# Kernel tuning notes

Hardware: AMD Instinct MI355X
Metric: run time of the kernel (lower is better)

The kernel has to match this reference:

```python
import jax, jax.numpy as jnp
import numpy as np

VOCAB, EMB, HID, OUT = 32000, 512, 1024, 1
B, S = 128, 512


def setup_inputs() -> dict:
    key = jax.random.key(0)
    ks = jax.random.split(key, 8)
    x = jax.random.randint(ks[0], (B, S), 0, VOCAB, dtype=jnp.int64 if jax.config.jax_enable_x64 else jnp.int32)
    emb = jax.random.normal(ks[1], (VOCAB, EMB), dtype=jnp.float32)
    # torch Linear stores weight as [out, in], y = x @ W.T + b
    W_w = jax.random.normal(ks[2], (HID, EMB), dtype=jnp.float32) * (1.0 / np.sqrt(EMB))
    W_b = jax.random.normal(ks[3], (HID,), dtype=jnp.float32) * 0.01
    U_w = jax.random.normal(ks[4], (HID, HID), dtype=jnp.float32) * (1.0 / np.sqrt(HID))
    U_b = jax.random.normal(ks[5], (HID,), dtype=jnp.float32) * 0.01
    V_w = jax.random.normal(ks[6], (OUT, HID), dtype=jnp.float32) * (1.0 / np.sqrt(HID))
    V_b = jax.random.normal(ks[7], (OUT,), dtype=jnp.float32) * 0.01
    return {"x": x, "emb": emb, "W_w": W_w, "W_b": W_b, "U_w": U_w, "U_b": U_b, "V_w": V_w, "V_b": V_b}


def reference(x, emb, W_w, W_b, U_w, U_b, V_w, V_b):
    xe = emb[x]  # [B, S, E] embedding lookup
    # Precompute input projection for all timesteps (same math as per-step W(x_t))
    pre = jnp.einsum('bse,he->bsh', xe, W_w) + W_b  # [B, S, H]

    def step(h, p_t):
        # h_t = tanh(W x_t + b_W + U h_{t-1} + b_U)
        h_new = jnp.tanh(p_t + h @ U_w.T + U_b)
        return h_new, None

    h0 = jnp.zeros((x.shape[0], U_w.shape[0]), dtype=pre.dtype)
    hT, _ = jax.lax.scan(step, h0, jnp.swapaxes(pre, 0, 1))  # scan over seq
    logits = hT @ V_w.T + V_b  # [B, OUT]
    return jax.nn.sigmoid(logits)
```

## Files before the change

kernel.cpp:

```cpp
#include <hip/hip_runtime.h>
#include <hip/hip_bf16.h>

typedef short short8 __attribute__((ext_vector_type(8)));
typedef float f32x4 __attribute__((ext_vector_type(4)));

#define OFF_U   0x0UL
#define OFF_W   0x200000UL
#define OFF_PRE 0x300000UL
#define OFF_H0  0x8300000UL
#define OFF_H1  0x8340000UL
#define OFF_CNT 0x8380000UL

static __device__ __forceinline__ unsigned short f2bf(float f) {
  return __builtin_bit_cast(unsigned short, __float2bfloat16(f));
}
static __device__ __forceinline__ float bf2f(unsigned short u) {
  unsigned int v = (unsigned int)u << 16;
  return __builtin_bit_cast(float, v);
}
static __device__ __forceinline__ unsigned int pack2(float a, float b) {
  return (unsigned int)f2bf(a) | ((unsigned int)f2bf(b) << 16);
}
static __device__ __forceinline__ float fast_tanh(float x) {
  float xc = fminf(fmaxf(x, -10.f), 10.f);
  float e2 = __expf(2.f * xc);
  return 1.f - 2.f * __builtin_amdgcn_rcpf(e2 + 1.f);
}

__global__ __launch_bounds__(256) void cvt_bf16(const float* __restrict__ in,
                                                unsigned short* __restrict__ out, int n4) {
  int idx = blockIdx.x * 256 + threadIdx.x;
  if (idx < n4) {
    float4 v = *(const float4*)&in[idx * 4];
    uint2 p; p.x = pack2(v.x, v.y); p.y = pack2(v.z, v.w);
    *(uint2*)&out[idx * 4] = p;
  }
}

__global__ __launch_bounds__(256) void pre_gemm(const int* __restrict__ x,
                                                const float* __restrict__ emb,
                                                const unsigned short* __restrict__ Wbf,
                                                unsigned short* __restrict__ pre) {
  const int t   = blockIdx.y;
  const int n0  = blockIdx.x * 128;
  const int tid = threadIdx.x;
  const int lane = tid & 63, w = tid >> 6;
  const int q = lane >> 4, l15 = lane & 15;

  __shared__ unsigned short Alds[128][72];
  __shared__ unsigned short Blds[128][72];
  __shared__ int tok[128];
  if (tid < 128) tok[tid] = x[tid * 512 + t];
  __syncthreads();

  f32x4 acc[4][4];
  #pragma unroll
  for (int a = 0; a < 4; ++a)
    #pragma unroll
    for (int b = 0; b < 4; ++b) acc[a][b] = {0.f, 0.f, 0.f, 0.f};

  const int wm = (w & 1) * 64, wn = (w >> 1) * 64;

  for (int k0 = 0; k0 < 512; k0 += 64) {
    #pragma unroll
    for (int it = 0; it < 8; ++it) {
      int idx = it * 256 + tid;
      int r = idx >> 4, c4 = (idx & 15) * 4;
      float4 v = *(const float4*)&emb[tok[r] * 512 + k0 + c4];
      uint2 p; p.x = pack2(v.x, v.y); p.y = pack2(v.z, v.w);
      *(uint2*)&Alds[r][c4] = p;
    }
    #pragma unroll
    for (int it = 0; it < 4; ++it) {
      int idx = it * 256 + tid;
      int r = idx >> 3, c8 = (idx & 7) * 8;
      *(int4*)&Blds[r][c8] = *(const int4*)&Wbf[(n0 + r) * 512 + k0 + c8];
    }
    __syncthreads();
    #pragma unroll
    for (int kt = 0; kt < 2; ++kt) {
      short8 af[4], bfr[4];
      #pragma unroll
      for (int mt = 0; mt < 4; ++mt) af[mt]  = *(const short8*)&Alds[wm + mt*16 + l15][kt*32 + q*8];
      #pragma unroll
      for (int nt = 0; nt < 4; ++nt) bfr[nt] = *(const short8*)&Blds[wn + nt*16 + l15][kt*32 + q*8];
      #pragma unroll
      for (int mt = 0; mt < 4; ++mt)
        #pragma unroll
        for (int nt = 0; nt < 4; ++nt)
          acc[mt][nt] = __builtin_amdgcn_mfma_f32_16x16x32_bf16(af[mt], bfr[nt], acc[mt][nt], 0, 0, 0);
    }
    __syncthreads();
  }
  #pragma unroll
  for (int mt = 0; mt < 4; ++mt) {
    int brow = wm + mt * 16 + q * 4;
    #pragma unroll
    for (int nt = 0; nt < 4; ++nt) {
      int i = n0 + wn + nt * 16 + l15;
      #pragma unroll
      for (int r = 0; r < 4; ++r)
        pre[(t * 128 + brow + r) * 1024 + i] = f2bf(acc[mt][nt][r]);
    }
  }
}

__global__ __launch_bounds__(512, 2) void recurrence(const unsigned short* __restrict__ Ubf,
                                                     const unsigned short* __restrict__ pre,
                                                     const float* __restrict__ Wb,
                                                     const float* __restrict__ Ub,
                                                     unsigned short* __restrict__ h0buf,
                                                     unsigned short* __restrict__ h1buf,
                                                     unsigned int* __restrict__ cnt) {
  const int c   = blockIdx.x & 7;
  const int s   = blockIdx.x >> 3;
  const int tid = threadIdx.x;
  const int lane = tid & 63, wv = tid >> 6;
  const int q = lane >> 4, l15 = lane & 15;
  const int ibase = s * 128 + wv * 16;
  const int bglob = c * 16;

  __shared__ unsigned short hlds[16][1032];

  short8 A[32];
  {
    const unsigned short* Up = Ubf + (ibase + l15) * 1024 + q * 8;
    #pragma unroll
    for (int kt = 0; kt < 32; ++kt) A[kt] = *(const short8*)(Up + kt * 32);
  }
  #pragma unroll
  for (int kt = 0; kt < 32; ++kt) asm volatile("" : "+v"(A[kt]));

  float4 bias;
  {
    int i0 = ibase + q * 4;
    float4 wb = *(const float4*)&Wb[i0];
    float4 ub = *(const float4*)&Ub[i0];
    bias = make_float4(wb.x + ub.x, wb.y + ub.y, wb.z + ub.z, wb.w + ub.w);
  }

  unsigned int* fbase = cnt + c * 32;
  const unsigned int* fpoll = fbase + (lane & 7);
  unsigned int* fmine = fbase + s;
  const int sb = tid >> 7;
  const int sk = (tid & 127) * 8;
  const unsigned short* prebase = pre + (size_t)(bglob + l15) * 1024 + ibase + q * 4;

  #pragma unroll 1
  for (int t = 0; t < 512; ++t) {
    ushort4 pv = *(const ushort4*)(prebase + (size_t)t * 131072);

    const unsigned short* hprev = (t & 1) ? h1buf : h0buf;
    unsigned short* hnew        = (t & 1) ? h0buf : h1buf;

    if (t > 0) {
      if (wv == 0) {
        const unsigned int tt = (unsigned int)t;
        for (;;) {
          unsigned int v;
          asm volatile("global_load_dword %0, %1, off sc1\n\ts_waitcnt vmcnt(0)"
                       : "=v"(v) : "v"(fpoll));
          if (__ballot(v < tt) == 0) break;
        }
      }
      __syncthreads();
    }

    {
      const unsigned short* hp = hprev + (size_t)(bglob + sb) * 1024 + sk;
      int4 r0, r1, r2, r3;
      asm volatile(
        "global_load_dwordx4 %0, %4, off sc1\n\t"
        "global_load_dwordx4 %1, %5, off sc1\n\t"
        "global_load_dwordx4 %2, %6, off sc1\n\t"
        "global_load_dwordx4 %3, %7, off sc1\n\t"
        "s_waitcnt vmcnt(0)"
        : "=&v"(r0), "=&v"(r1), "=&v"(r2), "=&v"(r3)
        : "v"(hp), "v"(hp + 4 * 1024), "v"(hp + 8 * 1024), "v"(hp + 12 * 1024));
      *(int4*)&hlds[sb][sk]      = r0;
      *(int4*)&hlds[sb + 4][sk]  = r1;
      *(int4*)&hlds[sb + 8][sk]  = r2;
      *(int4*)&hlds[sb + 12][sk] = r3;
    }
    __syncthreads();

    f32x4 acc0 = {0.f, 0.f, 0.f, 0.f}, acc1 = {0.f, 0.f, 0.f, 0.f};
    #pragma unroll
    for (int kt = 0; kt < 32; kt += 2) {
      short8 b0 = *(const short8*)&hlds[l15][kt * 32 + q * 8];
      short8 b1 = *(const short8*)&hlds[l15][kt * 32 + 32 + q * 8];
      acc0 = __builtin_amdgcn_mfma_f32_16x16x32_bf16(A[kt],     b0, acc0, 0, 0, 0);
      acc1 = __builtin_amdgcn_mfma_f32_16x16x32_bf16(A[kt + 1], b1, acc1, 0, 0, 0);
    }

    float x0 = acc0[0] + acc1[0] + bf2f(pv.x) + bias.x;
    float x1 = acc0[1] + acc1[1] + bf2f(pv.y) + bias.y;
    float x2 = acc0[2] + acc1[2] + bf2f(pv.z) + bias.z;
    float x3 = acc0[3] + acc1[3] + bf2f(pv.w) + bias.w;
    uint2 pk;
    pk.x = pack2(fast_tanh(x0), fast_tanh(x1));
    pk.y = pack2(fast_tanh(x2), fast_tanh(x3));

    {
      unsigned short* dst = hnew + (size_t)(bglob + l15) * 1024 + ibase + q * 4;
      asm volatile("global_store_dwordx2 %0, %1, off sc1\n\ts_waitcnt vmcnt(0)"
                   : : "v"(dst), "v"(pk));
    }
    __syncthreads();
    if (tid == 0) {
      unsigned int tv = (unsigned int)(t + 1);
      asm volatile("global_store_dword %0, %1, off sc1\n\ts_waitcnt vmcnt(0)"
                   : : "v"(fmine), "v"(tv));
    }
  }
}

__global__ __launch_bounds__(64) void final_out(const unsigned short* __restrict__ hT,
                                                const float* __restrict__ Vw,
                                                const float* __restrict__ Vb,
                                                float* __restrict__ out) {
  int b = blockIdx.x, lane = threadIdx.x;
  float sum = 0.f;
  #pragma unroll
  for (int k = 0; k < 16; ++k) {
    int i = k * 64 + lane;
    sum += bf2f(hT[b * 1024 + i]) * Vw[i];
  }
  #pragma unroll
  for (int off = 32; off; off >>= 1) sum += __shfl_down(sum, off);
  if (lane == 0) out[b] = 1.f / (1.f + expf(-(sum + Vb[0])));
}

extern "C" void kernel_launch(void* const* d_in, const int* in_sizes, int n_in,
                              void* d_out, int out_size, void* d_ws, size_t ws_size,
                              hipStream_t stream) {
  const int*   x   = (const int*)d_in[0];
  const float* emb = (const float*)d_in[1];
  const float* W_w = (const float*)d_in[2];
  const float* W_b = (const float*)d_in[3];
  const float* U_w = (const float*)d_in[4];
  const float* U_b = (const float*)d_in[5];
  const float* V_w = (const float*)d_in[6];
  const float* V_b = (const float*)d_in[7];
  float* out = (float*)d_out;
  char*  ws  = (char*)d_ws;

  unsigned short* Ubf = (unsigned short*)(ws + OFF_U);
  unsigned short* Wbf = (unsigned short*)(ws + OFF_W);
  unsigned short* pre = (unsigned short*)(ws + OFF_PRE);
  unsigned short* h0  = (unsigned short*)(ws + OFF_H0);
  unsigned short* h1  = (unsigned short*)(ws + OFF_H1);
  unsigned int*   cnt = (unsigned int*)(ws + OFF_CNT);

  hipMemsetAsync(ws + OFF_H0, 0, (OFF_CNT - OFF_H0) + 0x1000, stream);

  cvt_bf16<<<1024, 256, 0, stream>>>(U_w, Ubf, 1024 * 1024 / 4);
  cvt_bf16<<<512, 256, 0, stream>>>(W_w, Wbf, 1024 * 512 / 4);

  pre_gemm<<<dim3(8, 512), 256, 0, stream>>>(x, emb, Wbf, pre);

  void* args[] = {&Ubf, &pre, &W_b, &U_b, &h0, &h1, &cnt};
  hipLaunchCooperativeKernel((void*)recurrence, dim3(64), dim3(512), args, 0, stream);

  final_out<<<128, 64, 0, stream>>>(h0, V_w, V_b, out);
}
```

Measured before the change: 1.724 ms.

## Keep own h slice in LDS, pipeline flag polling, skip own-slice reload

Each block now writes its freshly computed h slice directly into LDS and reloads only the other blocks' slices from global memory. Flag polling skips the block's own flag and keeps two loads in flight instead of one. The pre load is issued early without waiting, and the final flag store no longer waits for completion. The goal is to shorten the per-timestep critical path of the cross-block recurrence. The cost is an extra __syncthreads per step, added so LDS is not overwritten while other waves still read it.

```diff
diff --git a/kernel.cpp b/kernel.cpp
--- a/kernel.cpp
+++ b/kernel.cpp
@@ -122,6 +122,12 @@
 
   __shared__ unsigned short hlds[16][1032];
 
+  {
+    int r = tid >> 5;
+    int kk = (tid & 31) * 4;
+    *(uint2*)&hlds[r][s * 128 + kk] = make_uint2(0u, 0u);
+  }
+
   short8 A[32];
   {
     const unsigned short* Up = Ubf + (ibase + l15) * 1024 + q * 8;
@@ -140,15 +146,23 @@
   }
 
   unsigned int* fbase = cnt + c * 32;
+  const bool pact = (lane < 8) && (lane != s);
   const unsigned int* fpoll = fbase + (lane & 7);
   unsigned int* fmine = fbase + s;
   const int sb = tid >> 7;
   const int sk = (tid & 127) * 8;
+  const bool notown = (sk >> 7) != s;
   const unsigned short* prebase = pre + (size_t)(bglob + l15) * 1024 + ibase + q * 4;
+
+  __syncthreads();
 
   #pragma unroll 1
   for (int t = 0; t < 512; ++t) {
-    ushort4 pv = *(const ushort4*)(prebase + (size_t)t * 131072);
+    uint2 pvr;
+    {
+      const unsigned short* pp = prebase + (size_t)t * 131072;
+      asm volatile("global_load_dwordx2 %0, %1, off" : "=v"(pvr) : "v"(pp));
+    }
 
     const unsigned short* hprev = (t & 1) ? h1buf : h0buf;
     unsigned short* hnew        = (t & 1) ? h0buf : h1buf;
@@ -156,12 +170,19 @@
     if (t > 0) {
       if (wv == 0) {
         const unsigned int tt = (unsigned int)t;
+        unsigned int va, vb;
+        asm volatile("global_load_dword %0, %1, off sc1" : "=v"(va) : "v"(fpoll));
         for (;;) {
-          unsigned int v;
-          asm volatile("global_load_dword %0, %1, off sc1\n\ts_waitcnt vmcnt(0)"
-                       : "=v"(v) : "v"(fpoll));
-          if (__ballot(v < tt) == 0) break;
+          asm volatile("global_load_dword %0, %1, off sc1\n\ts_waitcnt vmcnt(1)"
+                       : "=v"(vb) : "v"(fpoll));
+          unsigned int x = pact ? va : tt;
+          if (__ballot(x < tt) == 0) break;
+          asm volatile("global_load_dword %0, %1, off sc1\n\ts_waitcnt vmcnt(1)"
+                       : "=v"(va) : "v"(fpoll));
+          x = pact ? vb : tt;
+          if (__ballot(x < tt) == 0) break;
         }
+        asm volatile("s_waitcnt vmcnt(0)");
       }
       __syncthreads();
     }
@@ -169,18 +190,22 @@
     {
       const unsigned short* hp = hprev + (size_t)(bglob + sb) * 1024 + sk;
       int4 r0, r1, r2, r3;
-      asm volatile(
-        "global_load_dwordx4 %0, %4, off sc1\n\t"
-        "global_load_dwordx4 %1, %5, off sc1\n\t"
-        "global_load_dwordx4 %2, %6, off sc1\n\t"
-        "global_load_dwordx4 %3, %7, off sc1\n\t"
-        "s_waitcnt vmcnt(0)"
-        : "=&v"(r0), "=&v"(r1), "=&v"(r2), "=&v"(r3)
-        : "v"(hp), "v"(hp + 4 * 1024), "v"(hp + 8 * 1024), "v"(hp + 12 * 1024));
-      *(int4*)&hlds[sb][sk]      = r0;
-      *(int4*)&hlds[sb + 4][sk]  = r1;
-      *(int4*)&hlds[sb + 8][sk]  = r2;
-      *(int4*)&hlds[sb + 12][sk] = r3;
+      if (notown) {
+        asm volatile(
+          "global_load_dwordx4 %0, %4, off sc1\n\t"
+          "global_load_dwordx4 %1, %5, off sc1\n\t"
+          "global_load_dwordx4 %2, %6, off sc1\n\t"
+          "global_load_dwordx4 %3, %7, off sc1"
+          : "=&v"(r0), "=&v"(r1), "=&v"(r2), "=&v"(r3)
+          : "v"(hp), "v"(hp + 4 * 1024), "v"(hp + 8 * 1024), "v"(hp + 12 * 1024));
+      }
+      asm volatile("s_waitcnt vmcnt(0)");
+      if (notown) {
+        *(int4*)&hlds[sb][sk]      = r0;
+        *(int4*)&hlds[sb + 4][sk]  = r1;
+        *(int4*)&hlds[sb + 8][sk]  = r2;
+        *(int4*)&hlds[sb + 12][sk] = r3;
+      }
     }
     __syncthreads();
 
@@ -192,25 +217,31 @@
       acc0 = __builtin_amdgcn_mfma_f32_16x16x32_bf16(A[kt],     b0, acc0, 0, 0, 0);
       acc1 = __builtin_amdgcn_mfma_f32_16x16x32_bf16(A[kt + 1], b1, acc1, 0, 0, 0);
     }
-
-    float x0 = acc0[0] + acc1[0] + bf2f(pv.x) + bias.x;
-    float x1 = acc0[1] + acc1[1] + bf2f(pv.y) + bias.y;
-    float x2 = acc0[2] + acc1[2] + bf2f(pv.z) + bias.z;
-    float x3 = acc0[3] + acc1[3] + bf2f(pv.w) + bias.w;
+    __syncthreads();
+
+    float p0 = bf2f((unsigned short)(pvr.x & 0xffff));
+    float p1 = bf2f((unsigned short)(pvr.x >> 16));
+    float p2 = bf2f((unsigned short)(pvr.y & 0xffff));
+    float p3 = bf2f((unsigned short)(pvr.y >> 16));
+    float x0 = acc0[0] + acc1[0] + p0 + bias.x;
+    float x1 = acc0[1] + acc1[1] + p1 + bias.y;
+    float x2 = acc0[2] + acc1[2] + p2 + bias.z;
+    float x3 = acc0[3] + acc1[3] + p3 + bias.w;
     uint2 pk;
     pk.x = pack2(fast_tanh(x0), fast_tanh(x1));
     pk.y = pack2(fast_tanh(x2), fast_tanh(x3));
 
     {
-      unsigned short* dst = hnew + (size_t)(bglob + l15) * 1024 + ibase + q * 4;
+      const int i0 = ibase + q * 4;
+      *(uint2*)&hlds[l15][i0] = pk;
+      unsigned short* dst = hnew + (size_t)(bglob + l15) * 1024 + i0;
       asm volatile("global_store_dwordx2 %0, %1, off sc1\n\ts_waitcnt vmcnt(0)"
                    : : "v"(dst), "v"(pk));
     }
     __syncthreads();
     if (tid == 0) {
       unsigned int tv = (unsigned int)(t + 1);
-      asm volatile("global_store_dword %0, %1, off sc1\n\ts_waitcnt vmcnt(0)"
-                   : : "v"(fmine), "v"(tv));
+      asm volatile("global_store_dword %0, %1, off sc1" : : "v"(fmine), "v"(tv));
     }
   }
 }
```

Result: no change. 1.720 ms (-0.2%).
